# Kernel tuning notes

Measured on AMD Instinct MI355X. Metric: run time of the kernel, lower is better.

The kernel has to match this reference:

```python
import jax, jax.numpy as jnp
import numpy as np

IN_CH, OUT_CH, K, STRIDE = 128, 256, 3, 1

def setup_inputs() -> dict:
    key = jax.random.key(0)
    kx, kw = jax.random.split(key)
    x = jax.random.normal(kx, (32, IN_CH, 56, 56), dtype=jnp.float32)
    # xavier_uniform: bound = sqrt(6 / (fan_in + fan_out)), fans include receptive field
    fan_in = IN_CH * K * K
    fan_out = OUT_CH * K * K
    bound = float(np.sqrt(6.0 / (fan_in + fan_out)))
    weight = jax.random.uniform(kw, (OUT_CH, IN_CH, K, K), dtype=jnp.float32,
                                minval=-bound, maxval=bound)
    bias = jnp.zeros((OUT_CH,), dtype=jnp.float32)
    return {"x": x, "weight": weight, "bias": bias}

def reference(x, weight, bias):
    # VALID (no-padding) conv, stride STRIDE, NCHW layout, OIHW kernel
    out = jax.lax.conv_general_dilated(
        x, weight,
        window_strides=(STRIDE, STRIDE),
        padding="VALID",
        dimension_numbers=("NCHW", "OIHW", "NCHW"))
    return out + bias[None, :, None, None]
```

## Files before the change

### kernel.cpp

```cpp
#include <hip/hip_runtime.h>
#include <hip/hip_bf16.h>
#include <stdint.h>

#define NB    32
#define CIN   128
#define HIN   56
#define HW    (HIN*HIN)
#define OCH   256
#define OHW   54
#define SPB   (OHW*OHW)
#define KSZ   (CIN*9)
#define BM    128
#define BN    256
#define BK    64
#define NKS   (KSZ/BK)
#define TOTC  (NB*SPB)
#define NT    365

typedef __attribute__((ext_vector_type(8))) short bf16x8;
typedef __attribute__((ext_vector_type(4))) float f32x4;

typedef __attribute__((address_space(1))) const uint32_t g_u32;
typedef __attribute__((address_space(3))) uint32_t l_u32;
static __device__ __forceinline__ void gl_lds16(const void* g, void* l) {
    __builtin_amdgcn_global_load_lds((g_u32*)g, (l_u32*)l, 16, 0, 0);
}

__global__ void xpose_cast(const float* __restrict__ x, __hip_bfloat16* __restrict__ xt) {
    __shared__ float tile[32][33];
    const int hw0 = blockIdx.x * 32;
    const int c0  = blockIdx.y * 32;
    const int n   = blockIdx.z;
    const int tx = threadIdx.x, ty = threadIdx.y;
    const float* xp = x + ((size_t)n*CIN + c0)*HW + hw0;
    #pragma unroll
    for (int i = ty; i < 32; i += 8)
        tile[i][tx] = xp[(size_t)i*HW + tx];
    __syncthreads();
    const int t = ty*32 + tx;
    const int hwl = t >> 3, q = t & 7;
    ushort4 v;
    v.x = __bfloat16_as_ushort(__float2bfloat16(tile[q*4+0][hwl]));
    v.y = __bfloat16_as_ushort(__float2bfloat16(tile[q*4+1][hwl]));
    v.z = __bfloat16_as_ushort(__float2bfloat16(tile[q*4+2][hwl]));
    v.w = __bfloat16_as_ushort(__float2bfloat16(tile[q*4+3][hwl]));
    __hip_bfloat16* op = xt + ((size_t)n*HW + hw0 + hwl)*CIN + c0 + q*4;
    *(ushort4*)op = v;
}

__global__ void wcast(const float* __restrict__ w, __hip_bfloat16* __restrict__ wt) {
    int tid = blockIdx.x*256 + threadIdx.x;
    if (tid >= OCH*KSZ) return;
    int oc = tid / KSZ, r = tid % KSZ;
    int pos = r >> 7, ic = r & 127;
    wt[tid] = __float2bfloat16(w[((size_t)(oc*CIN + ic))*9 + pos]);
}

__global__ __launch_bounds__(512, 2)
void conv_mfma(const __hip_bfloat16* __restrict__ xt,
               const __hip_bfloat16* __restrict__ wt,
               const float* __restrict__ bias,
               float* __restrict__ out) {
    __shared__ uint4 smem[3*3072];

    const int t = threadIdx.x;
    const int tile = blockIdx.x, octile = blockIdx.y;
    const int lane = t & 63, wid = t >> 6;
    const int wm = wid >> 2, wn = wid & 3;
    const int lr = lane & 15, lq = lane >> 4;

    const __hip_bfloat16* asrc[2];
    #pragma unroll
    for (int i = 0; i < 2; ++i) {
        int p = i*512 + t;
        int row = p >> 3, g = (p & 7) ^ (row & 7);
        asrc[i] = wt + (size_t)(octile*BM + row)*KSZ + g*8;
    }
    const __hip_bfloat16* bsrc[4];
    #pragma unroll
    for (int i = 0; i < 4; ++i) {
        int p = i*512 + t;
        int row = p >> 3, g = (p & 7) ^ (row & 7);
        int colg = tile*BN + row; if (colg >= TOTC) colg = TOTC - 1;
        int n = colg / SPB, rem = colg - n*SPB;
        int oh = rem / OHW, ow = rem - oh*OHW;
        bsrc[i] = xt + ((size_t)(n*HIN + oh)*HIN + ow)*CIN + g*8;
    }

    auto issue = [&](int ks, int part) {
        uint4* Ab = smem + (ks % 3)*3072;
        uint4* Bb = Ab + 1024;
        const int pos = ks >> 1;
        const int kh = pos / 3, kw = pos - kh*3;
        const int aoff = ks*BK;
        const int boff = (kh*HIN + kw)*CIN + (ks & 1)*64;
        if (part == 0) {
            gl_lds16(asrc[0] + aoff, Ab + t);
            gl_lds16(asrc[1] + aoff, Ab + 512 + t);
            gl_lds16(bsrc[0] + boff, Bb + t);
        } else {
            gl_lds16(bsrc[1] + boff, Bb + 512 + t);
            gl_lds16(bsrc[2] + boff, Bb + 1024 + t);
            gl_lds16(bsrc[3] + boff, Bb + 1536 + t);
        }
    };

    f32x4 acc[4][4];
    #pragma unroll
    for (int i = 0; i < 4; ++i)
        #pragma unroll
        for (int j = 0; j < 4; ++j)
            acc[i][j] = (f32x4){0.f, 0.f, 0.f, 0.f};

    issue(0, 0); issue(0, 1);
    issue(1, 0); issue(1, 1);

    for (int ks = 0; ks < NKS; ++ks) {
        if (ks < NKS-1) asm volatile("s_waitcnt vmcnt(6)" ::: "memory");
        else            asm volatile("s_waitcnt vmcnt(0)" ::: "memory");
        __builtin_amdgcn_s_barrier();
        __builtin_amdgcn_sched_barrier(0);

        const uint4* Ab = smem + (ks % 3)*3072;
        const uint4* Bb = Ab + 1024;

        #pragma unroll
        for (int kk = 0; kk < 2; ++kk) {
            if (ks + 2 < NKS) issue(ks + 2, kk);
            bf16x8 a[4], b[4];
            #pragma unroll
            for (int mi = 0; mi < 4; ++mi) {
                int ra = wm*64 + mi*16 + lr;
                a[mi] = *(bf16x8*)&Ab[ra*8 + ((kk*4 + lq) ^ (ra & 7))];
            }
            #pragma unroll
            for (int ni = 0; ni < 4; ++ni) {
                int rb = wn*64 + ni*16 + lr;
                b[ni] = *(bf16x8*)&Bb[rb*8 + ((kk*4 + lq) ^ (rb & 7))];
            }
            __builtin_amdgcn_s_setprio(1);
            #pragma unroll
            for (int mi = 0; mi < 4; ++mi)
                #pragma unroll
                for (int ni = 0; ni < 4; ++ni)
                    acc[mi][ni] = __builtin_amdgcn_mfma_f32_16x16x32_bf16(
                        a[mi], b[ni], acc[mi][ni], 0, 0, 0);
            __builtin_amdgcn_s_setprio(0);
        }
    }

    __syncthreads();

    float (*eps)[264] = (float (*)[264])smem;
    for (int h = 0; h < 2; ++h) {
        if (wm == h) {
            #pragma unroll
            for (int mi = 0; mi < 4; ++mi) {
                int rl = mi*16 + lq*4;
                #pragma unroll
                for (int ni = 0; ni < 4; ++ni) {
                    int cl = wn*64 + ni*16 + lr;
                    #pragma unroll
                    for (int r = 0; r < 4; ++r)
                        eps[rl + r][cl] = acc[mi][ni][r];
                }
            }
        }
        __syncthreads();
        const int cl4 = (t & 63) * 4;
        const int rsub = t >> 6;
        const int colg = tile*BN + cl4;
        if (colg < TOTC) {
            const int n = colg / SPB;
            const int sp = colg - n*SPB;
            #pragma unroll
            for (int pass = 0; pass < 8; ++pass) {
                int rl = pass*8 + rsub;
                int rg = octile*BM + h*64 + rl;
                f32x4 v = *(f32x4*)&eps[rl][cl4];
                v = v + bias[rg];
                *(f32x4*)&out[((size_t)n*OCH + rg)*SPB + sp] = v;
            }
        }
        __syncthreads();
    }
}

__global__ void conv_naive(const float* __restrict__ x, const float* __restrict__ w,
                           const float* __restrict__ bias, float* __restrict__ out) {
    size_t tid = (size_t)blockIdx.x*256 + threadIdx.x;
    const size_t total = (size_t)NB*OCH*SPB;
    if (tid >= total) return;
    int col = (int)(tid % SPB);
    int oc  = (int)((tid / SPB) % OCH);
    int n   = (int)(tid / ((size_t)SPB*OCH));
    int oh = col / OHW, ow = col % OHW;
    float s = bias[oc];
    for (int ic = 0; ic < CIN; ++ic)
        #pragma unroll
        for (int kh = 0; kh < 3; ++kh)
            #pragma unroll
            for (int kw = 0; kw < 3; ++kw)
                s += x[((size_t)(n*CIN+ic)*HIN + oh+kh)*HIN + ow+kw]
                   * w[((size_t)(oc*CIN+ic)*3 + kh)*3 + kw];
    out[tid] = s;
}

extern "C" void kernel_launch(void* const* d_in, const int* in_sizes, int n_in,
                              void* d_out, int out_size, void* d_ws, size_t ws_size,
                              hipStream_t stream) {
    const float* x    = (const float*)d_in[0];
    const float* w    = (const float*)d_in[1];
    const float* bias = (const float*)d_in[2];
    float* out = (float*)d_out;

    const size_t xt_bytes = (size_t)NB*HW*CIN*sizeof(__hip_bfloat16);
    const size_t wt_bytes = (size_t)OCH*KSZ*sizeof(__hip_bfloat16);

    if (ws_size >= xt_bytes + wt_bytes) {
        __hip_bfloat16* xt  = (__hip_bfloat16*)d_ws;
        __hip_bfloat16* wtp = (__hip_bfloat16*)((char*)d_ws + xt_bytes);
        hipLaunchKernelGGL(xpose_cast, dim3(HW/32, CIN/32, NB), dim3(32, 8), 0, stream, x, xt);
        hipLaunchKernelGGL(wcast, dim3((OCH*KSZ + 255)/256), dim3(256), 0, stream, w, wtp);
        hipLaunchKernelGGL(conv_mfma, dim3(NT, OCH/BM), dim3(512), 0, stream,
                           xt, wtp, bias, out);
    } else {
        size_t total = (size_t)NB*OCH*SPB;
        hipLaunchKernelGGL(conv_naive, dim3((unsigned)((total + 255)/256)), dim3(256), 0, stream,
                           x, w, bias, out);
    }
}
```

Baseline: 89.26 us.

## Split main loop into four barrier-synchronized phases interleaving LDS reads, prefetch, and MFMA

Restructures the K-step loop into four sub-phases, each reading part of the A/B fragments from LDS, issuing a third of the next-next-stage global-to-LDS loads, and running eight MFMAs between workgroup barriers, in a ping-pong style schedule. Global loads are regrouped into three units and the vmcnt wait moves to the end of the iteration. The aim is finer-grained overlap of memory traffic with MFMA across the two co-resident blocks. It adds many extra barriers per iteration, which may cost more than the overlap gains. The epilogue staging stride also changes from 264 to 260 floats.

```diff
diff --git a/kernel.cpp b/kernel.cpp
--- a/kernel.cpp
+++ b/kernel.cpp
@@ -87,19 +87,20 @@
         bsrc[i] = xt + ((size_t)(n*HIN + oh)*HIN + ow)*CIN + g*8;
     }
 
-    auto issue = [&](int ks, int part) {
+    auto issueU = [&](int ks, int unit) {
         uint4* Ab = smem + (ks % 3)*3072;
         uint4* Bb = Ab + 1024;
         const int pos = ks >> 1;
         const int kh = pos / 3, kw = pos - kh*3;
         const int aoff = ks*BK;
         const int boff = (kh*HIN + kw)*CIN + (ks & 1)*64;
-        if (part == 0) {
+        if (unit == 0) {
             gl_lds16(asrc[0] + aoff, Ab + t);
             gl_lds16(asrc[1] + aoff, Ab + 512 + t);
+        } else if (unit == 1) {
             gl_lds16(bsrc[0] + boff, Bb + t);
+            gl_lds16(bsrc[1] + boff, Bb + 512 + t);
         } else {
-            gl_lds16(bsrc[1] + boff, Bb + 512 + t);
             gl_lds16(bsrc[2] + boff, Bb + 1024 + t);
             gl_lds16(bsrc[3] + boff, Bb + 1536 + t);
         }
@@ -112,46 +113,91 @@
         for (int j = 0; j < 4; ++j)
             acc[i][j] = (f32x4){0.f, 0.f, 0.f, 0.f};
 
-    issue(0, 0); issue(0, 1);
-    issue(1, 0); issue(1, 1);
+    issueU(0,0); issueU(0,1); issueU(0,2);
+    issueU(1,0); issueU(1,1); issueU(1,2);
+    asm volatile("s_waitcnt vmcnt(6)" ::: "memory");
+    __builtin_amdgcn_s_barrier();
+
+    #define MFMA_BF16 __builtin_amdgcn_mfma_f32_16x16x32_bf16
 
     for (int ks = 0; ks < NKS; ++ks) {
-        if (ks < NKS-1) asm volatile("s_waitcnt vmcnt(6)" ::: "memory");
-        else            asm volatile("s_waitcnt vmcnt(0)" ::: "memory");
-        __builtin_amdgcn_s_barrier();
-        __builtin_amdgcn_sched_barrier(0);
-
         const uint4* Ab = smem + (ks % 3)*3072;
         const uint4* Bb = Ab + 1024;
-
-        #pragma unroll
-        for (int kk = 0; kk < 2; ++kk) {
-            if (ks + 2 < NKS) issue(ks + 2, kk);
-            bf16x8 a[4], b[4];
-            #pragma unroll
-            for (int mi = 0; mi < 4; ++mi) {
-                int ra = wm*64 + mi*16 + lr;
-                a[mi] = *(bf16x8*)&Ab[ra*8 + ((kk*4 + lq) ^ (ra & 7))];
-            }
-            #pragma unroll
-            for (int ni = 0; ni < 4; ++ni) {
-                int rb = wn*64 + ni*16 + lr;
-                b[ni] = *(bf16x8*)&Bb[rb*8 + ((kk*4 + lq) ^ (rb & 7))];
-            }
-            __builtin_amdgcn_s_setprio(1);
-            #pragma unroll
-            for (int mi = 0; mi < 4; ++mi)
-                #pragma unroll
-                for (int ni = 0; ni < 4; ++ni)
-                    acc[mi][ni] = __builtin_amdgcn_mfma_f32_16x16x32_bf16(
-                        a[mi], b[ni], acc[mi][ni], 0, 0, 0);
-            __builtin_amdgcn_s_setprio(0);
-        }
+        bf16x8 a0[4], a1[4], bA, bB, bC, bD;
+
+        #pragma unroll
+        for (int mi = 0; mi < 4; ++mi) {
+            int ra = wm*64 + mi*16 + lr;
+            a0[mi] = *(bf16x8*)&Ab[ra*8 + (lq ^ (ra & 7))];
+        }
+        { int rb = wn*64 +  0 + lr; bA = *(bf16x8*)&Bb[rb*8 + (lq ^ (rb & 7))]; }
+        { int rb = wn*64 + 16 + lr; bB = *(bf16x8*)&Bb[rb*8 + (lq ^ (rb & 7))]; }
+        if (ks + 2 < NKS) issueU(ks + 2, 0);
+        __builtin_amdgcn_s_barrier();
+        asm volatile("s_waitcnt lgkmcnt(0)");
+        __builtin_amdgcn_s_setprio(1);
+        #pragma unroll
+        for (int mi = 0; mi < 4; ++mi) {
+            acc[mi][0] = MFMA_BF16(a0[mi], bA, acc[mi][0], 0, 0, 0);
+            acc[mi][1] = MFMA_BF16(a0[mi], bB, acc[mi][1], 0, 0, 0);
+        }
+        __builtin_amdgcn_s_setprio(0);
+        __builtin_amdgcn_s_barrier();
+
+        { int rb = wn*64 + 32 + lr; bC = *(bf16x8*)&Bb[rb*8 + (lq ^ (rb & 7))]; }
+        { int rb = wn*64 + 48 + lr; bD = *(bf16x8*)&Bb[rb*8 + (lq ^ (rb & 7))]; }
+        if (ks + 2 < NKS) issueU(ks + 2, 1);
+        __builtin_amdgcn_s_barrier();
+        asm volatile("s_waitcnt lgkmcnt(0)");
+        __builtin_amdgcn_s_setprio(1);
+        #pragma unroll
+        for (int mi = 0; mi < 4; ++mi) {
+            acc[mi][2] = MFMA_BF16(a0[mi], bC, acc[mi][2], 0, 0, 0);
+            acc[mi][3] = MFMA_BF16(a0[mi], bD, acc[mi][3], 0, 0, 0);
+        }
+        __builtin_amdgcn_s_setprio(0);
+        __builtin_amdgcn_s_barrier();
+
+        #pragma unroll
+        for (int mi = 0; mi < 4; ++mi) {
+            int ra = wm*64 + mi*16 + lr;
+            a1[mi] = *(bf16x8*)&Ab[ra*8 + ((4 + lq) ^ (ra & 7))];
+        }
+        { int rb = wn*64 +  0 + lr; bA = *(bf16x8*)&Bb[rb*8 + ((4 + lq) ^ (rb & 7))]; }
+        { int rb = wn*64 + 16 + lr; bB = *(bf16x8*)&Bb[rb*8 + ((4 + lq) ^ (rb & 7))]; }
+        if (ks + 2 < NKS) issueU(ks + 2, 2);
+        __builtin_amdgcn_s_barrier();
+        asm volatile("s_waitcnt lgkmcnt(0)");
+        __builtin_amdgcn_s_setprio(1);
+        #pragma unroll
+        for (int mi = 0; mi < 4; ++mi) {
+            acc[mi][0] = MFMA_BF16(a1[mi], bA, acc[mi][0], 0, 0, 0);
+            acc[mi][1] = MFMA_BF16(a1[mi], bB, acc[mi][1], 0, 0, 0);
+        }
+        __builtin_amdgcn_s_setprio(0);
+        __builtin_amdgcn_s_barrier();
+
+        { int rb = wn*64 + 32 + lr; bC = *(bf16x8*)&Bb[rb*8 + ((4 + lq) ^ (rb & 7))]; }
+        { int rb = wn*64 + 48 + lr; bD = *(bf16x8*)&Bb[rb*8 + ((4 + lq) ^ (rb & 7))]; }
+        __builtin_amdgcn_s_barrier();
+        asm volatile("s_waitcnt lgkmcnt(0)");
+        __builtin_amdgcn_s_setprio(1);
+        #pragma unroll
+        for (int mi = 0; mi < 4; ++mi) {
+            acc[mi][2] = MFMA_BF16(a1[mi], bC, acc[mi][2], 0, 0, 0);
+            acc[mi][3] = MFMA_BF16(a1[mi], bD, acc[mi][3], 0, 0, 0);
+        }
+        __builtin_amdgcn_s_setprio(0);
+        if (ks < NKS-1) {
+            if (ks == NKS-2) asm volatile("s_waitcnt vmcnt(0)" ::: "memory");
+            else             asm volatile("s_waitcnt vmcnt(6)" ::: "memory");
+        }
+        __builtin_amdgcn_s_barrier();
     }
 
     __syncthreads();
 
-    float (*eps)[264] = (float (*)[264])smem;
+    float (*eps)[260] = (float (*)[260])smem;
     for (int h = 0; h < 2; ++h) {
         if (wm == h) {
             #pragma unroll
```

Result: slower. 100.8 us (+13.0%).

## Widen conv GEMM tile to all output channels with double-buffered phased MFMA schedule

Applied to the files above, without the earlier changes.

Makes each block cover the full set of 256 output channels (BM 128→256), so the input patch tile is read once per spatial tile instead of twice and the grid drops to 365 blocks. The three-stage LDS ring is replaced by a 2-stage double buffer (128 KiB LDS), with the next tile loaded whole while compute runs. Each k-step is split into four barrier-separated phases of LDS reads plus 16 MFMAs. Per-thread accumulators double to 128 floats, which hurts occupancy, and 365 blocks on 256 CUs leaves a partial second wave.

```diff
diff --git a/kernel.cpp b/kernel.cpp
--- a/kernel.cpp
+++ b/kernel.cpp
@@ -10,7 +10,7 @@
 #define OHW   54
 #define SPB   (OHW*OHW)
 #define KSZ   (CIN*9)
-#define BM    128
+#define BM    256
 #define BN    256
 #define BK    64
 #define NKS   (KSZ/BK)
@@ -61,125 +61,137 @@
                const __hip_bfloat16* __restrict__ wt,
                const float* __restrict__ bias,
                float* __restrict__ out) {
-    __shared__ uint4 smem[3*3072];
+    __shared__ uint4 smem[8192];
 
     const int t = threadIdx.x;
-    const int tile = blockIdx.x, octile = blockIdx.y;
+    const int tile = blockIdx.x;
     const int lane = t & 63, wid = t >> 6;
     const int wm = wid >> 2, wn = wid & 3;
     const int lr = lane & 15, lq = lane >> 4;
 
-    const __hip_bfloat16* asrc[2];
-    #pragma unroll
-    for (int i = 0; i < 2; ++i) {
-        int p = i*512 + t;
-        int row = p >> 3, g = (p & 7) ^ (row & 7);
-        asrc[i] = wt + (size_t)(octile*BM + row)*KSZ + g*8;
-    }
+    const __hip_bfloat16* asrc[4];
     const __hip_bfloat16* bsrc[4];
     #pragma unroll
     for (int i = 0; i < 4; ++i) {
         int p = i*512 + t;
         int row = p >> 3, g = (p & 7) ^ (row & 7);
+        asrc[i] = wt + (size_t)row*KSZ + g*8;
         int colg = tile*BN + row; if (colg >= TOTC) colg = TOTC - 1;
         int n = colg / SPB, rem = colg - n*SPB;
         int oh = rem / OHW, ow = rem - oh*OHW;
         bsrc[i] = xt + ((size_t)(n*HIN + oh)*HIN + ow)*CIN + g*8;
     }
 
-    auto issue = [&](int ks, int part) {
-        uint4* Ab = smem + (ks % 3)*3072;
-        uint4* Bb = Ab + 1024;
+    auto issueTile = [&](int ks) {
+        uint4* Ab = smem + (ks & 1)*4096;
+        uint4* Bb = Ab + 2048;
         const int pos = ks >> 1;
         const int kh = pos / 3, kw = pos - kh*3;
         const int aoff = ks*BK;
         const int boff = (kh*HIN + kw)*CIN + (ks & 1)*64;
-        if (part == 0) {
-            gl_lds16(asrc[0] + aoff, Ab + t);
-            gl_lds16(asrc[1] + aoff, Ab + 512 + t);
-            gl_lds16(bsrc[0] + boff, Bb + t);
-        } else {
-            gl_lds16(bsrc[1] + boff, Bb + 512 + t);
-            gl_lds16(bsrc[2] + boff, Bb + 1024 + t);
-            gl_lds16(bsrc[3] + boff, Bb + 1536 + t);
-        }
+        #pragma unroll
+        for (int i = 0; i < 4; ++i) gl_lds16(asrc[i] + aoff, Ab + i*512 + t);
+        #pragma unroll
+        for (int i = 0; i < 4; ++i) gl_lds16(bsrc[i] + boff, Bb + i*512 + t);
     };
 
-    f32x4 acc[4][4];
-    #pragma unroll
-    for (int i = 0; i < 4; ++i)
+    f32x4 acc[8][4];
+    #pragma unroll
+    for (int i = 0; i < 8; ++i)
         #pragma unroll
         for (int j = 0; j < 4; ++j)
             acc[i][j] = (f32x4){0.f, 0.f, 0.f, 0.f};
 
-    issue(0, 0); issue(0, 1);
-    issue(1, 0); issue(1, 1);
+    issueTile(0);
+    asm volatile("s_waitcnt vmcnt(0)" ::: "memory");
+    __builtin_amdgcn_s_barrier();
+
+    #define MFMA_BF16 __builtin_amdgcn_mfma_f32_16x16x32_bf16
+    #define RD_A(dst, MIB, KK) \
+        { int ra = wm*128 + (MIB)*16 + lr; \
+          dst = *(bf16x8*)&Ab[ra*8 + (((KK)*4 + lq) ^ (ra & 7))]; }
+    #define RD_B(dst, NI, KK) \
+        { int rb = wn*64 + (NI)*16 + lr; \
+          dst = *(bf16x8*)&Bb[rb*8 + (((KK)*4 + lq) ^ (rb & 7))]; }
+    #define PH_SYNC() \
+        __builtin_amdgcn_s_barrier(); \
+        asm volatile("s_waitcnt lgkmcnt(0)"); \
+        __builtin_amdgcn_sched_barrier(0);
+    #define MFMA16(AARR, MIB, BARR) \
+        __builtin_amdgcn_s_setprio(1); \
+        _Pragma("unroll") \
+        for (int ii = 0; ii < 4; ++ii) \
+            _Pragma("unroll") \
+            for (int ni = 0; ni < 4; ++ni) \
+                acc[(MIB)+ii][ni] = MFMA_BF16(AARR[ii], BARR[ni], acc[(MIB)+ii][ni], 0, 0, 0); \
+        __builtin_amdgcn_s_setprio(0); \
+        __builtin_amdgcn_s_barrier();
 
     for (int ks = 0; ks < NKS; ++ks) {
-        if (ks < NKS-1) asm volatile("s_waitcnt vmcnt(6)" ::: "memory");
-        else            asm volatile("s_waitcnt vmcnt(0)" ::: "memory");
+        const uint4* Ab = smem + (ks & 1)*4096;
+        const uint4* Bb = Ab + 2048;
+        bf16x8 a[4], b[4];
+
+        RD_A(a[0], 0, 0) RD_A(a[1], 1, 0) RD_A(a[2], 2, 0) RD_A(a[3], 3, 0)
+        RD_B(b[0], 0, 0) RD_B(b[1], 1, 0) RD_B(b[2], 2, 0) RD_B(b[3], 3, 0)
+        if (ks + 1 < NKS) issueTile(ks + 1);
+        PH_SYNC()
+        MFMA16(a, 0, b)
+
+        RD_A(a[0], 4, 0) RD_A(a[1], 5, 0) RD_A(a[2], 6, 0) RD_A(a[3], 7, 0)
+        PH_SYNC()
+        MFMA16(a, 4, b)
+
+        RD_A(a[0], 0, 1) RD_A(a[1], 1, 1) RD_A(a[2], 2, 1) RD_A(a[3], 3, 1)
+        RD_B(b[0], 0, 1) RD_B(b[1], 1, 1) RD_B(b[2], 2, 1) RD_B(b[3], 3, 1)
+        PH_SYNC()
+        MFMA16(a, 0, b)
+
+        RD_A(a[0], 4, 1) RD_A(a[1], 5, 1) RD_A(a[2], 6, 1) RD_A(a[3], 7, 1)
+        PH_SYNC()
+        __builtin_amdgcn_s_setprio(1);
+        #pragma unroll
+        for (int ii = 0; ii < 4; ++ii)
+            #pragma unroll
+            for (int ni = 0; ni < 4; ++ni)
+                acc[4+ii][ni] = MFMA_BF16(a[ii], b[ni], acc[4+ii][ni], 0, 0, 0);
+        __builtin_amdgcn_s_setprio(0);
+        if (ks + 1 < NKS)
+            asm volatile("s_waitcnt vmcnt(0)" ::: "memory");
         __builtin_amdgcn_s_barrier();
-        __builtin_amdgcn_sched_barrier(0);
-
-        const uint4* Ab = smem + (ks % 3)*3072;
-        const uint4* Bb = Ab + 1024;
-
-        #pragma unroll
-        for (int kk = 0; kk < 2; ++kk) {
-            if (ks + 2 < NKS) issue(ks + 2, kk);
-            bf16x8 a[4], b[4];
-            #pragma unroll
-            for (int mi = 0; mi < 4; ++mi) {
-                int ra = wm*64 + mi*16 + lr;
-                a[mi] = *(bf16x8*)&Ab[ra*8 + ((kk*4 + lq) ^ (ra & 7))];
-            }
-            #pragma unroll
-            for (int ni = 0; ni < 4; ++ni) {
-                int rb = wn*64 + ni*16 + lr;
-                b[ni] = *(bf16x8*)&Bb[rb*8 + ((kk*4 + lq) ^ (rb & 7))];
-            }
-            __builtin_amdgcn_s_setprio(1);
-            #pragma unroll
-            for (int mi = 0; mi < 4; ++mi)
-                #pragma unroll
-                for (int ni = 0; ni < 4; ++ni)
-                    acc[mi][ni] = __builtin_amdgcn_mfma_f32_16x16x32_bf16(
-                        a[mi], b[ni], acc[mi][ni], 0, 0, 0);
-            __builtin_amdgcn_s_setprio(0);
-        }
-    }
-
-    __syncthreads();
-
-    float (*eps)[264] = (float (*)[264])smem;
-    for (int h = 0; h < 2; ++h) {
-        if (wm == h) {
-            #pragma unroll
-            for (int mi = 0; mi < 4; ++mi) {
-                int rl = mi*16 + lq*4;
+    }
+
+    float (*eps)[260] = (float (*)[260])smem;
+    const int cl4 = (t & 63) * 4;
+    const int rsub = t >> 6;
+    const int colg = tile*BN + cl4;
+    int nn = 0, sp = 0;
+    if (colg < TOTC) { nn = colg / SPB; sp = colg - nn*SPB; }
+    #pragma unroll
+    for (int h = 0; h < 4; ++h) {
+        if (wm == (h >> 1)) {
+            const int mib = (h & 1) * 4;
+            #pragma unroll
+            for (int ii = 0; ii < 4; ++ii) {
+                int rl = ii*16 + lq*4;
                 #pragma unroll
                 for (int ni = 0; ni < 4; ++ni) {
                     int cl = wn*64 + ni*16 + lr;
                     #pragma unroll
                     for (int r = 0; r < 4; ++r)
-                        eps[rl + r][cl] = acc[mi][ni][r];
+                        eps[rl + r][cl] = acc[mib + ii][ni][r];
                 }
             }
         }
         __syncthreads();
-        const int cl4 = (t & 63) * 4;
-        const int rsub = t >> 6;
-        const int colg = tile*BN + cl4;
         if (colg < TOTC) {
-            const int n = colg / SPB;
-            const int sp = colg - n*SPB;
             #pragma unroll
             for (int pass = 0; pass < 8; ++pass) {
                 int rl = pass*8 + rsub;
-                int rg = octile*BM + h*64 + rl;
+                int rg = h*64 + rl;
                 f32x4 v = *(f32x4*)&eps[rl][cl4];
                 v = v + bias[rg];
-                *(f32x4*)&out[((size_t)n*OCH + rg)*SPB + sp] = v;
+                *(f32x4*)&out[((size_t)nn*OCH + rg)*SPB + sp] = v;
             }
         }
         __syncthreads();
@@ -222,8 +234,7 @@
         __hip_bfloat16* wtp = (__hip_bfloat16*)((char*)d_ws + xt_bytes);
         hipLaunchKernelGGL(xpose_cast, dim3(HW/32, CIN/32, NB), dim3(32, 8), 0, stream, x, xt);
         hipLaunchKernelGGL(wcast, dim3((OCH*KSZ + 255)/256), dim3(256), 0, stream, w, wtp);
-        hipLaunchKernelGGL(conv_mfma, dim3(NT, OCH/BM), dim3(512), 0, stream,
-                           xt, wtp, bias, out);
+        hipLaunchKernelGGL(conv_mfma, dim3(NT), dim3(512), 0, stream, xt, wtp, bias, out);
     } else {
         size_t total = (size_t)NB*OCH*SPB;
         hipLaunchKernelGGL(conv_naive, dim3((unsigned)((total + 255)/256)), dim3(256), 0, stream,
```

Result: slower. 101.3 us (+13.5%).
